# Kernel optimization log

Hardware: AMD Instinct MI355X
Metric: run time of the kernel (lower is better)

Reference implementation:

```python
import jax, jax.numpy as jnp
import numpy as np

QMIN, QMAX = 0.0, 255.0
# activation statistics (min, max) per layer, from init_kwargs['stats']
STATS = {"conv1": (-0.5, 3.0), "conv2": (0.0, 6.0), "fc1": (0.0, 8.0), "fc2": (0.0, 10.0)}


def calc_scale_zp(min_val, max_val):
    scale = (max_val - min_val) / (QMAX - QMIN)
    # original: int(clamped initial zero point) -> truncation
    zp = jnp.trunc(jnp.clip(QMIN - min_val / scale, QMIN, QMAX))
    return scale, zp


def quantize(x, min_val=None, max_val=None):
    if min_val is None:
        min_val, max_val = x.min(), x.max()
    scale, zp = calc_scale_zp(min_val, max_val)
    q = jnp.round(jnp.clip(zp + x / scale, QMIN, QMAX))
    return q, scale, zp


def conv2d(x, w, b):
    y = jax.lax.conv_general_dilated(x, w, (1, 1), "VALID",
                                     dimension_numbers=("NCHW", "OIHW", "NCHW"))
    return y + b[None, :, None, None]


def linear(x, w, b):
    return x @ w.T + b


def max_pool_2x2(x):
    return jax.lax.reduce_window(x, -jnp.inf, jax.lax.max, (1, 1, 2, 2), (1, 1, 2, 2), "VALID")


def quantize_layer(q_x, scale_x, zp_x, W, B, apply_fn, stat):
    # fake-quant weights/bias with their own min/max
    wq, scale_w, zp_w = quantize(W)
    bq, scale_b, zp_b = quantize(B)
    scale_next, zp_next = calc_scale_zp(stat[0], stat[1])
    X = q_x - zp_x
    W_eff = scale_x * scale_w * (wq - zp_w)
    B_eff = scale_b * (bq + zp_b)  # '+ zp_b' is faithful to the source
    y = jax.nn.relu(apply_fn(X, W_eff, B_eff) / scale_next + zp_next)
    # .round().byte() in torch wraps mod 256
    return jnp.mod(jnp.round(y), 256.0), scale_next, zp_next


def setup_inputs() -> dict:
    key = jax.random.key(0)
    ks = jax.random.split(key, 9)
    B = 4096
    return {
        "x": jax.random.normal(ks[0], (B, 1, 28, 28), jnp.float32),
        "conv1_w": jax.random.normal(ks[1], (20, 1, 5, 5), jnp.float32) * 0.1,
        "conv1_b": jax.random.normal(ks[2], (20,), jnp.float32) * 0.1,
        "conv2_w": jax.random.normal(ks[3], (50, 20, 5, 5), jnp.float32) * 0.05,
        "conv2_b": jax.random.normal(ks[4], (50,), jnp.float32) * 0.05,
        "fc1_w": jax.random.normal(ks[5], (500, 800), jnp.float32) * 0.03,
        "fc1_b": jax.random.normal(ks[6], (500,), jnp.float32) * 0.03,
        "fc2_w": jax.random.normal(ks[7], (10, 500), jnp.float32) * 0.05,
        "fc2_b": jax.random.normal(ks[8], (10,), jnp.float32) * 0.05,
    }


def reference(x, conv1_w, conv1_b, conv2_w, conv2_b, fc1_w, fc1_b, fc2_w, fc2_b):
    q, s, zp = quantize(x, STATS["conv1"][0], STATS["conv1"][1])
    q, s, zp = quantize_layer(q, s, zp, conv1_w, conv1_b, conv2d, STATS["conv2"])
    q = max_pool_2x2(q)                       # [B,20,12,12]
    q, s, zp = quantize_layer(q, s, zp, conv2_w, conv2_b, conv2d, STATS["fc1"])
    q = max_pool_2x2(q)                       # [B,50,4,4]
    q = q.reshape(-1, 4 * 4 * 50)             # [B,800]
    q, s, zp = quantize_layer(q, s, zp, fc1_w, fc1_b, linear, STATS["fc2"])
    xf = s * (q - zp)                         # dequantize
    logits = linear(xf, fc2_w, fc2_b)         # [B,10]
    return jax.nn.log_softmax(logits, axis=1)
```

## Files before the change

kernel.cpp:

```cpp
#include <hip/hip_runtime.h>
#include <cmath>

#define TPB 256
typedef float floatx4 __attribute__((ext_vector_type(4)));
typedef __bf16 bf16x8 __attribute__((ext_vector_type(8)));
typedef unsigned short ushort8 __attribute__((ext_vector_type(8)));
typedef unsigned short ushort_t;

#define OFF_PMN 16
#define OFF_PMX 96
#define OFF_B1 520
#define OFF_B2 544
#define OFF_B3 600
#define W1BF_BYTE 6144
#define W2BF_BYTE 8192
#define W3BF_BYTE 131072
#define Q2_BYTE  29360128ULL
#define Q3_BYTE  1048576ULL

#define S_X1 (3.5f/255.0f)
#define ZP_X1 36.0f
#define S_N1 (6.0f/255.0f)
#define S_N2 (8.0f/255.0f)
#define S_N3 (10.0f/255.0f)

#define XSTR 40

__device__ inline float qclip(float x, float s, float zp){
    return rintf(fminf(fmaxf(zp + x / s, 0.0f), 255.0f));
}
__device__ inline ushort_t bfbits(float v){
    return (ushort_t)(__float_as_uint(v) >> 16);
}

__global__ __launch_bounds__(TPB) void k_minmax(
        const float* c1w, const float* c1b, const float* c2w, const float* c2b,
        const float* f1w, const float* f1b, float* pmn, float* pmx){
    __shared__ float smn[TPB], smx[TPB];
    int bb = blockIdx.x, tid = threadIdx.x;
    const float* src; int n, sub, nsub;
    if      (bb == 0){ src=c1w; n=500;    sub=0;     nsub=1;  }
    else if (bb == 1){ src=c1b; n=20;     sub=0;     nsub=1;  }
    else if (bb <  6){ src=c2w; n=25000;  sub=bb-2;  nsub=4;  }
    else if (bb == 6){ src=c2b; n=50;     sub=0;     nsub=1;  }
    else if (bb < 71){ src=f1w; n=400000; sub=bb-7;  nsub=64; }
    else             { src=f1b; n=500;    sub=0;     nsub=1;  }
    float mn = INFINITY, mx = -INFINITY;
    for (int i = sub*TPB + tid; i < n; i += nsub*TPB){
        float v = src[i]; mn = fminf(mn, v); mx = fmaxf(mx, v);
    }
    smn[tid] = mn; smx[tid] = mx; __syncthreads();
    for (int s = TPB/2; s > 0; s >>= 1){
        if (tid < s){
            smn[tid] = fminf(smn[tid], smn[tid+s]);
            smx[tid] = fmaxf(smx[tid], smx[tid+s]);
        }
        __syncthreads();
    }
    if (tid == 0){ pmn[bb] = smn[0]; pmx[bb] = smx[0]; }
}

#define N_EFF 452157
__global__ __launch_bounds__(TPB) void k_make_eff(
        const float* c1w, const float* c1b, const float* c2w, const float* c2b,
        const float* f1w, const float* f1b, const float* pmn, const float* pmx,
        float* ws, ushort_t* w1bf, ushort_t* w2bf, ushort_t* w3bf){
    __shared__ float sS[6], sZ[6];
    int tid = threadIdx.x;
    int wv = tid >> 6, lane = tid & 63;
    const int starts[6] = {0,1,2,6,7,71};
    const int counts[6] = {1,1,4,1,64,1};
    #pragma unroll
    for (int rep = 0; rep < 2; ++rep){
        int t = wv + rep*4;
        if (t < 6){
            float mn = INFINITY, mx = -INFINITY;
            if (lane < counts[t]){ mn = pmn[starts[t]+lane]; mx = pmx[starts[t]+lane]; }
            #pragma unroll
            for (int off = 32; off > 0; off >>= 1){
                mn = fminf(mn, __shfl_xor(mn, off));
                mx = fmaxf(mx, __shfl_xor(mx, off));
            }
            if (lane == 0){
                float s = (mx - mn) / 255.0f;
                sS[t] = s;
                sZ[t] = truncf(fminf(fmaxf(0.0f - mn / s, 0.0f), 255.0f));
            }
        }
    }
    __syncthreads();

    int i = blockIdx.x * TPB + tid;
    if (i >= N_EFF) return;
    if (i < 1024){
        int n = i >> 5, k = i & 31;
        float v = 0.0f;
        if (n < 20 && k < 25) v = qclip(c1w[n*25 + k], sS[0], sZ[0]) - sZ[0];
        w1bf[i] = bfbits(v);
    } else if (i < 1044){
        int j = i - 1024;
        ws[OFF_B1 + j] = (sS[1] * (qclip(c1b[j], sS[1], sZ[1]) + sZ[1])) / S_N1;
    } else if (i < 42004){
        int j = i - 1044;
        int c = j >> 11, r = j & 2047, co = r >> 5, k = r & 31;
        int q = k >> 3, jj = k & 7;
        int tap, ci; bool valid;
        if (c < 13){ tap = 2*c + (q>>1); ci = (q&1)*8 + jj; valid = (tap < 25); }
        else       { tap = 4*(c-13) + q; ci = 16 + jj;      valid = (tap < 25) && (jj < 4); }
        valid = valid && (co < 50);
        float v = 0.0f;
        if (valid) v = qclip(c2w[(co*20 + ci)*25 + tap], sS[2], sZ[2]) - sZ[2];
        w2bf[j] = bfbits(v);
    } else if (i < 42054){
        int j = i - 42004;
        ws[OFF_B2 + j] = (sS[3] * (qclip(c2b[j], sS[3], sZ[3]) + sZ[3])) / S_N2;
    } else if (i < 451654){
        int j = i - 42054;
        int n = j / 800, k = j - 800*n;
        float v = 0.0f;
        if (n < 500) v = qclip(f1w[n*800 + k], sS[4], sZ[4]) - sZ[4];
        w3bf[j] = bfbits(v);
    } else if (i < 452154){
        int j = i - 451654;
        ws[OFF_B3 + j] = (sS[5] * (qclip(f1b[j], sS[5], sZ[5]) + sZ[5])) / S_N3;
    } else if (i == 452154){
        ws[0] = (S_N1 * sS[2]) / S_N2;
    } else if (i == 452155){
        ws[1] = (S_N2 * sS[4]) / S_N3;
    } else {
        ws[2] = (S_X1 * sS[0]) / S_N1;
    }
}

__global__ __launch_bounds__(TPB) void k_conv12(const float* x, const ushort_t* w1bf,
                                                const ushort_t* w2bt, const float* ws,
                                                ushort_t* q2bf, int B){
    __shared__ __align__(16) ushort_t xs[144*XSTR];
    __shared__ __align__(16) ushort_t xim[3136];
    int b = blockIdx.x, tid = threadIdx.x;
    int lane = tid & 63, wv = tid >> 6;
    int ln = lane & 15, quad = lane >> 4;

    for (int i = tid; i < 144; i += TPB){
        *(unsigned int*)(xs + i*XSTR + 20) = 0u;
        *(unsigned int*)(xs + i*XSTR + 22) = 0u;
    }

    const float* xb = x + (size_t)b * 784;
    for (int i = tid; i < 784; i += TPB){
        float v = xb[i];
        float q = rintf(fminf(fmaxf(ZP_X1 + v / S_X1, 0.0f), 255.0f));
        ushort_t bits = bfbits(q - ZP_X1);
        xim[i] = bits; xim[784 + i] = bits; xim[1568 + i] = bits; xim[2352 + i] = bits;
    }

    int offj[8]; bool vj[8];
    #pragma unroll
    for (int j = 0; j < 8; ++j){
        int k = quad*8 + j;
        vj[j] = (k < 25);
        int kh = k / 5, kw = k - 5*kh;
        offj[j] = vj[j] ? (kh*28 + kw) : 0;
    }
    const ushort_t* xq = xim + quad*784;

    ushort8 bw0 = *(const ushort8*)(w1bf + ln*32 + quad*8);
    ushort8 bw1 = *(const ushort8*)(w1bf + (16 + ln)*32 + quad*8);
    bf16x8 bf0 = __builtin_bit_cast(bf16x8, bw0);
    bf16x8 bf1 = __builtin_bit_cast(bf16x8, bw1);

    float K1 = ws[2];
    float B1_0 = ws[OFF_B1 + ln];
    float B1_1 = (ln < 4) ? ws[OFF_B1 + 16 + ln] : 0.0f;
    __syncthreads();

    for (int i = 0; i < 9; ++i){
        int mt = 9*wv + i;
        int m = mt*16 + ln;
        int p = m >> 2, crn = m & 3;
        int ph_ = p / 12, pw_ = p - 12*ph_;
        int oh = 2*ph_ + (crn >> 1), ow = 2*pw_ + (crn & 1);
        int base = oh*28 + ow;
        ushort8 aw;
        #pragma unroll
        for (int j = 0; j < 8; ++j)
            aw[j] = vj[j] ? xq[base + offj[j]] : (ushort_t)0;
        bf16x8 af = __builtin_bit_cast(bf16x8, aw);
        floatx4 z = (floatx4){0.f,0.f,0.f,0.f};
        floatx4 a0 = __builtin_amdgcn_mfma_f32_16x16x32_bf16(af, bf0, z, 0, 0, 0);
        floatx4 a1 = __builtin_amdgcn_mfma_f32_16x16x32_bf16(af, bf1, z, 0, 0, 0);

        int pp = mt*4 + quad;
        {
            unsigned int qv[4];
            #pragma unroll
            for (int r = 0; r < 4; ++r){
                float y = fmaxf(fmaf(a0[r], K1, B1_0), 0.0f);
                qv[r] = ((unsigned int)rintf(y)) & 255u;
            }
            unsigned int h0 = qv[0] > qv[1] ? qv[0] : qv[1];
            unsigned int h1 = qv[2] > qv[3] ? qv[2] : qv[3];
            unsigned int mx = h0 > h1 ? h0 : h1;
            xs[pp*XSTR + ln] = bfbits((float)mx);
        }
        if (ln < 4){
            unsigned int qv[4];
            #pragma unroll
            for (int r = 0; r < 4; ++r){
                float y = fmaxf(fmaf(a1[r], K1, B1_1), 0.0f);
                qv[r] = ((unsigned int)rintf(y)) & 255u;
            }
            unsigned int h0 = qv[0] > qv[1] ? qv[0] : qv[1];
            unsigned int h1 = qv[2] > qv[3] ? qv[2] : qv[3];
            unsigned int mx = h0 > h1 ? h0 : h1;
            xs[pp*XSTR + 16 + ln] = bfbits((float)mx);
        }
    }
    __syncthreads();

    int mt0 = (wv & 1) * 2;
    int nt0 = (wv >> 1) * 2;
    int abase[2];
    #pragma unroll
    for (int mi = 0; mi < 2; ++mi)
        abase[mi] = (24*(mt0+mi) + (ln>>3)*12 + (ln&7)) * XSTR;
    int aoff[20];
    #pragma unroll
    for (int c = 0; c < 20; ++c){
        int tap, inner;
        if (c < 13){ tap = 2*c + (quad>>1); inner = (quad&1)*8; }
        else       { tap = 4*(c-13) + quad; inner = 16; }
        int pt = 0;
        if (tap < 25){ int kh = tap/5, kw = tap-5*kh; pt = kh*12 + kw; }
        aoff[c] = pt*XSTR + inner;
    }

    float sc2d = ws[0];
    const ushort_t* bsrc0 = w2bt + (size_t)(nt0*16 + ln)*32 + quad*8;
    const ushort_t* bsrc1 = bsrc0 + 16*32;

    floatx4 acc[2][2];
    #pragma unroll
    for (int mi = 0; mi < 2; ++mi)
        #pragma unroll
        for (int ni = 0; ni < 2; ++ni) acc[mi][ni] = (floatx4){0.f,0.f,0.f,0.f};

    #pragma unroll
    for (int c = 0; c < 20; ++c){
        ushort8 b0w = *(const ushort8*)(bsrc0 + c*2048);
        ushort8 b1w = *(const ushort8*)(bsrc1 + c*2048);
        ushort8 a0w = *(const ushort8*)(xs + abase[0] + aoff[c]);
        ushort8 a1w = *(const ushort8*)(xs + abase[1] + aoff[c]);
        bf16x8 a0 = __builtin_bit_cast(bf16x8, a0w);
        bf16x8 a1 = __builtin_bit_cast(bf16x8, a1w);
        bf16x8 b0 = __builtin_bit_cast(bf16x8, b0w);
        bf16x8 b1 = __builtin_bit_cast(bf16x8, b1w);
        acc[0][0] = __builtin_amdgcn_mfma_f32_16x16x32_bf16(a0, b0, acc[0][0], 0, 0, 0);
        acc[0][1] = __builtin_amdgcn_mfma_f32_16x16x32_bf16(a0, b1, acc[0][1], 0, 0, 0);
        acc[1][0] = __builtin_amdgcn_mfma_f32_16x16x32_bf16(a1, b0, acc[1][0], 0, 0, 0);
        acc[1][1] = __builtin_amdgcn_mfma_f32_16x16x32_bf16(a1, b1, acc[1][1], 0, 0, 0);
    }

    #pragma unroll
    for (int ni = 0; ni < 2; ++ni){
        int co = (nt0 + ni)*16 + ln;
        float bias2d = (co < 50) ? ws[OFF_B2 + co] : 0.0f;
        #pragma unroll
        for (int mi = 0; mi < 2; ++mi){
            int mt = mt0 + mi;
            unsigned int qv[4];
            #pragma unroll
            for (int r = 0; r < 4; ++r){
                float y = fmaxf(fmaf(acc[mi][ni][r], sc2d, bias2d), 0.0f);
                qv[r] = ((unsigned int)rintf(y)) & 255u;
            }
            unsigned int h0 = qv[0] > qv[1] ? qv[0] : qv[1];
            unsigned int h1 = qv[2] > qv[3] ? qv[2] : qv[3];
            unsigned int p0 = (unsigned int)__shfl_xor((int)h0, 32);
            unsigned int p1 = (unsigned int)__shfl_xor((int)h1, 32);
            unsigned int v0 = h0 > p0 ? h0 : p0;
            unsigned int v1 = h1 > p1 ? h1 : p1;
            if (quad < 2 && co < 50){
                size_t base = (size_t)b*800 + co*16 + mt*4 + quad*2;
                q2bf[base]     = bfbits((float)v0);
                q2bf[base + 1] = bfbits((float)v1);
            }
        }
    }
}

__global__ __launch_bounds__(TPB) void k_fc1(const ushort_t* q2bf, const ushort_t* w3bf,
                                             const float* ws, unsigned char* q3, int B){
    int tid = threadIdx.x;
    int lane = tid & 63, wv = tid >> 6;
    int ln = lane & 15, quad = lane >> 4;
    int n0 = blockIdx.x * 64 + wv*16;
    int b0 = blockIdx.y * 32;

    const ushort_t* bsrc = w3bf + (size_t)(n0 + ln)*800 + quad*8;
    const ushort_t* asrc0 = q2bf + (size_t)(b0 + ln)*800 + quad*8;
    const ushort_t* asrc1 = q2bf + (size_t)(b0 + 16 + ln)*800 + quad*8;

    floatx4 acc[2];
    #pragma unroll
    for (int mt = 0; mt < 2; ++mt) acc[mt] = (floatx4){0.f,0.f,0.f,0.f};

    #pragma unroll
    for (int c = 0; c < 25; ++c){
        ushort8 bw  = *(const ushort8*)(bsrc  + c*32);
        ushort8 a0w = *(const ushort8*)(asrc0 + c*32);
        ushort8 a1w = *(const ushort8*)(asrc1 + c*32);
        bf16x8 bfr = __builtin_bit_cast(bf16x8, bw);
        acc[0] = __builtin_amdgcn_mfma_f32_16x16x32_bf16(
                     __builtin_bit_cast(bf16x8, a0w), bfr, acc[0], 0, 0, 0);
        acc[1] = __builtin_amdgcn_mfma_f32_16x16x32_bf16(
                     __builtin_bit_cast(bf16x8, a1w), bfr, acc[1], 0, 0, 0);
    }

    float sc3d = ws[1];
    int n = n0 + ln;
    if (n < 500){
        float bias = ws[OFF_B3 + n];
        #pragma unroll
        for (int mt = 0; mt < 2; ++mt){
            #pragma unroll
            for (int r = 0; r < 4; ++r){
                int m = 16*mt + 4*quad + r;
                float y = fmaxf(fmaf(acc[mt][r], sc3d, bias), 0.0f);
                q3[(size_t)(b0 + m)*500 + n] = (unsigned char)(((unsigned int)rintf(y)) & 255u);
            }
        }
    }
}

__global__ __launch_bounds__(TPB) void k_fc2(const unsigned char* q3, const float* w2,
                                             const float* b2, float* out, int B){
    int tid = threadIdx.x;
    int lane = tid & 63, wv = tid >> 6;
    int b = blockIdx.x*4 + wv;
    if (b >= B) return;
    float acc[10];
    #pragma unroll
    for (int c = 0; c < 10; ++c) acc[c] = 0.0f;
    #pragma unroll
    for (int it = 0; it < 8; ++it){
        int k = lane + it*64;
        if (k < 500){
            float xf = S_N3 * (float)q3[(size_t)b*500 + k];
            #pragma unroll
            for (int c = 0; c < 10; ++c)
                acc[c] = fmaf(xf, w2[c*500 + k], acc[c]);
        }
    }
    #pragma unroll
    for (int off = 32; off > 0; off >>= 1)
        #pragma unroll
        for (int c = 0; c < 10; ++c)
            acc[c] += __shfl_xor(acc[c], off);
    float lg[10], m = -INFINITY;
    #pragma unroll
    for (int c = 0; c < 10; ++c){ lg[c] = acc[c] + b2[c]; m = fmaxf(m, lg[c]); }
    float sum = 0.0f;
    #pragma unroll
    for (int c = 0; c < 10; ++c) sum += expf(lg[c] - m);
    float ls = logf(sum);
    if (lane < 10) out[(size_t)b*10 + lane] = lg[lane] - m - ls;
}

extern "C" void kernel_launch(void* const* d_in, const int* in_sizes, int n_in,
                              void* d_out, int out_size, void* d_ws, size_t ws_size,
                              hipStream_t stream){
    const float* x   = (const float*)d_in[0];
    const float* c1w = (const float*)d_in[1];
    const float* c1b = (const float*)d_in[2];
    const float* c2w = (const float*)d_in[3];
    const float* c2b = (const float*)d_in[4];
    const float* f1w = (const float*)d_in[5];
    const float* f1b = (const float*)d_in[6];
    const float* f2w = (const float*)d_in[7];
    const float* f2b = (const float*)d_in[8];
    int B = in_sizes[0] / 784;

    float* ws = (float*)d_ws;
    float* pmn = ws + OFF_PMN;
    float* pmx = ws + OFF_PMX;
    ushort_t* w1bf = (ushort_t*)((char*)d_ws + W1BF_BYTE);
    ushort_t* w2bf = (ushort_t*)((char*)d_ws + W2BF_BYTE);
    ushort_t* w3bf = (ushort_t*)((char*)d_ws + W3BF_BYTE);
    ushort_t* q2bf = (ushort_t*)((char*)d_ws + Q2_BYTE);
    unsigned char* q3 = (unsigned char*)d_ws + Q3_BYTE;
    float* out = (float*)d_out;

    k_minmax<<<72, TPB, 0, stream>>>(c1w, c1b, c2w, c2b, f1w, f1b, pmn, pmx);
    k_make_eff<<<(N_EFF + TPB - 1)/TPB, TPB, 0, stream>>>(c1w, c1b, c2w, c2b, f1w, f1b, pmn, pmx, ws, w1bf, w2bf, w3bf);
    k_conv12<<<B, TPB, 0, stream>>>(x, w1bf, w2bf, ws, q2bf, B);
    dim3 g_fc1(8, (B + 31)/32);
    k_fc1<<<g_fc1, TPB, 0, stream>>>(q2bf, w3bf, ws, q3, B);
    k_fc2<<<(B + 3)/4, TPB, 0, stream>>>(q3, f2w, f2b, out, B);
}
```

Measured before the change: 161.6 us.

## Fuse fc1 and fc2 with log-softmax into one kernel

Merges the fc1 MFMA GEMM and the fc2 plus log-softmax kernel into a single kernel. Each 512-thread block handles 16 batch rows across all 512 (padded) fc1 outputs, requantizes in registers, and does the fc2 dot products with shuffles and a shared-memory reduction. This removes the q3 intermediate round trip through global memory and one kernel launch. In exchange each block reloads the full fc1 weight matrix and runs only 256 blocks, with the B-side loads no longer reused across two M tiles. It also assumes B is a multiple of 16.

```diff
diff --git a/kernel.cpp b/kernel.cpp
--- a/kernel.cpp
+++ b/kernel.cpp
@@ -16,7 +16,6 @@
 #define W2BF_BYTE 8192
 #define W3BF_BYTE 131072
 #define Q2_BYTE  29360128ULL
-#define Q3_BYTE  1048576ULL
 
 #define S_X1 (3.5f/255.0f)
 #define ZP_X1 36.0f
@@ -289,82 +288,87 @@
     }
 }
 
-__global__ __launch_bounds__(TPB) void k_fc1(const ushort_t* q2bf, const ushort_t* w3bf,
-                                             const float* ws, unsigned char* q3, int B){
+__global__ __launch_bounds__(512) void k_fc12(const ushort_t* q2bf, const ushort_t* w3bf,
+                                              const float* ws, const float* w2,
+                                              const float* b2, float* out, int B){
+    __shared__ float red[8*16*10];
     int tid = threadIdx.x;
     int lane = tid & 63, wv = tid >> 6;
     int ln = lane & 15, quad = lane >> 4;
-    int n0 = blockIdx.x * 64 + wv*16;
-    int b0 = blockIdx.y * 32;
-
-    const ushort_t* bsrc = w3bf + (size_t)(n0 + ln)*800 + quad*8;
-    const ushort_t* asrc0 = q2bf + (size_t)(b0 + ln)*800 + quad*8;
-    const ushort_t* asrc1 = q2bf + (size_t)(b0 + 16 + ln)*800 + quad*8;
-
-    floatx4 acc[2];
-    #pragma unroll
-    for (int mt = 0; mt < 2; ++mt) acc[mt] = (floatx4){0.f,0.f,0.f,0.f};
-
-    #pragma unroll
+    int b0 = blockIdx.x * 16;
+
+    const ushort_t* asrc = q2bf + (size_t)(b0 + ln)*800 + quad*8;
+
+    floatx4 acc[4];
+    #pragma unroll
+    for (int t = 0; t < 4; ++t) acc[t] = (floatx4){0.f,0.f,0.f,0.f};
+
     for (int c = 0; c < 25; ++c){
-        ushort8 bw  = *(const ushort8*)(bsrc  + c*32);
-        ushort8 a0w = *(const ushort8*)(asrc0 + c*32);
-        ushort8 a1w = *(const ushort8*)(asrc1 + c*32);
-        bf16x8 bfr = __builtin_bit_cast(bf16x8, bw);
-        acc[0] = __builtin_amdgcn_mfma_f32_16x16x32_bf16(
-                     __builtin_bit_cast(bf16x8, a0w), bfr, acc[0], 0, 0, 0);
-        acc[1] = __builtin_amdgcn_mfma_f32_16x16x32_bf16(
-                     __builtin_bit_cast(bf16x8, a1w), bfr, acc[1], 0, 0, 0);
+        ushort8 aw = *(const ushort8*)(asrc + c*32);
+        bf16x8 af = __builtin_bit_cast(bf16x8, aw);
+        #pragma unroll
+        for (int t = 0; t < 4; ++t){
+            int n = wv*64 + t*16 + ln;
+            ushort8 bw = *(const ushort8*)(w3bf + (size_t)n*800 + c*32 + quad*8);
+            acc[t] = __builtin_amdgcn_mfma_f32_16x16x32_bf16(
+                         af, __builtin_bit_cast(bf16x8, bw), acc[t], 0, 0, 0);
+        }
     }
 
     float sc3d = ws[1];
-    int n = n0 + ln;
-    if (n < 500){
-        float bias = ws[OFF_B3 + n];
-        #pragma unroll
-        for (int mt = 0; mt < 2; ++mt){
-            #pragma unroll
-            for (int r = 0; r < 4; ++r){
-                int m = 16*mt + 4*quad + r;
-                float y = fmaxf(fmaf(acc[mt][r], sc3d, bias), 0.0f);
-                q3[(size_t)(b0 + m)*500 + n] = (unsigned char)(((unsigned int)rintf(y)) & 255u);
-            }
-        }
-    }
-}
-
-__global__ __launch_bounds__(TPB) void k_fc2(const unsigned char* q3, const float* w2,
-                                             const float* b2, float* out, int B){
-    int tid = threadIdx.x;
-    int lane = tid & 63, wv = tid >> 6;
-    int b = blockIdx.x*4 + wv;
-    if (b >= B) return;
-    float acc[10];
-    #pragma unroll
-    for (int c = 0; c < 10; ++c) acc[c] = 0.0f;
-    #pragma unroll
-    for (int it = 0; it < 8; ++it){
-        int k = lane + it*64;
-        if (k < 500){
-            float xf = S_N3 * (float)q3[(size_t)b*500 + k];
-            #pragma unroll
-            for (int c = 0; c < 10; ++c)
-                acc[c] = fmaf(xf, w2[c*500 + k], acc[c]);
-        }
-    }
-    #pragma unroll
-    for (int off = 32; off > 0; off >>= 1)
+    float xf[4][4];
+    #pragma unroll
+    for (int t = 0; t < 4; ++t){
+        int col = wv*64 + t*16 + ln;
+        float bias = (col < 500) ? ws[OFF_B3 + col] : 0.0f;
+        #pragma unroll
+        for (int r = 0; r < 4; ++r){
+            float y = fmaxf(fmaf(acc[t][r], sc3d, bias), 0.0f);
+            unsigned int q = ((unsigned int)rintf(y)) & 255u;
+            xf[r][t] = (col < 500) ? S_N3 * (float)q : 0.0f;
+        }
+    }
+
+    #pragma unroll
+    for (int c = 0; c < 10; ++c){
+        float p[4] = {0.f, 0.f, 0.f, 0.f};
+        #pragma unroll
+        for (int t = 0; t < 4; ++t){
+            int col = wv*64 + t*16 + ln;
+            float w = (col < 500) ? w2[c*500 + col] : 0.0f;
+            #pragma unroll
+            for (int r = 0; r < 4; ++r) p[r] = fmaf(xf[r][t], w, p[r]);
+        }
+        #pragma unroll
+        for (int m = 1; m <= 8; m <<= 1)
+            #pragma unroll
+            for (int r = 0; r < 4; ++r) p[r] += __shfl_xor(p[r], m);
+        if (ln == 0){
+            #pragma unroll
+            for (int r = 0; r < 4; ++r)
+                red[(wv*16 + quad*4 + r)*10 + c] = p[r];
+        }
+    }
+    __syncthreads();
+
+    if (tid < 16){
+        int row = tid;
+        float lg[10], mx = -INFINITY;
+        #pragma unroll
+        for (int c = 0; c < 10; ++c){
+            float s = b2[c];
+            #pragma unroll
+            for (int w = 0; w < 8; ++w) s += red[(w*16 + row)*10 + c];
+            lg[c] = s; mx = fmaxf(mx, s);
+        }
+        float sum = 0.0f;
+        #pragma unroll
+        for (int c = 0; c < 10; ++c) sum += expf(lg[c] - mx);
+        float ls = logf(sum);
         #pragma unroll
         for (int c = 0; c < 10; ++c)
-            acc[c] += __shfl_xor(acc[c], off);
-    float lg[10], m = -INFINITY;
-    #pragma unroll
-    for (int c = 0; c < 10; ++c){ lg[c] = acc[c] + b2[c]; m = fmaxf(m, lg[c]); }
-    float sum = 0.0f;
-    #pragma unroll
-    for (int c = 0; c < 10; ++c) sum += expf(lg[c] - m);
-    float ls = logf(sum);
-    if (lane < 10) out[(size_t)b*10 + lane] = lg[lane] - m - ls;
+            out[(size_t)(b0 + row)*10 + c] = lg[c] - mx - ls;
+    }
 }
 
 extern "C" void kernel_launch(void* const* d_in, const int* in_sizes, int n_in,
@@ -388,13 +392,10 @@
     ushort_t* w2bf = (ushort_t*)((char*)d_ws + W2BF_BYTE);
     ushort_t* w3bf = (ushort_t*)((char*)d_ws + W3BF_BYTE);
     ushort_t* q2bf = (ushort_t*)((char*)d_ws + Q2_BYTE);
-    unsigned char* q3 = (unsigned char*)d_ws + Q3_BYTE;
     float* out = (float*)d_out;
 
     k_minmax<<<72, TPB, 0, stream>>>(c1w, c1b, c2w, c2b, f1w, f1b, pmn, pmx);
     k_make_eff<<<(N_EFF + TPB - 1)/TPB, TPB, 0, stream>>>(c1w, c1b, c2w, c2b, f1w, f1b, pmn, pmx, ws, w1bf, w2bf, w3bf);
     k_conv12<<<B, TPB, 0, stream>>>(x, w1bf, w2bf, ws, q2bf, B);
-    dim3 g_fc1(8, (B + 31)/32);
-    k_fc1<<<g_fc1, TPB, 0, stream>>>(q2bf, w3bf, ws, q3, B);
-    k_fc2<<<(B + 3)/4, TPB, 0, stream>>>(q3, f2w, f2b, out, B);
-}
+    k_fc12<<<B/16, 512, 0, stream>>>(q2bf, w3bf, ws, f2w, f2b, out, B);
+}
```

Measured after the change: 159.3 us. Within noise of the previous version (-1.4%).
